# Kernel tuning notes

Measured on AMD Instinct MI355X. Metric: run time of the kernel, lower is better.

Reference implementation:

```python
import jax, jax.numpy as jnp
import numpy as np

DIM = 128   # EMBED_DIM
NH = 4      # N_HEADS
HD = DIM // NH          # 32
NT = max(1, int(NH * 0.25))  # 1 timelike head
NS = NH - NT                 # 3 spacelike heads
TD = NT * HD                 # T_DIM = 32
SD = 6      # STATE_DIM
TIN, TOUT = 20, 20
NL = 3      # N_LAYERS
B, T = 4096, TIN + TOUT      # seq len capped by pos embedding (40)


def _ln(x, g, b):
    m = jnp.mean(x, -1, keepdims=True)
    v = jnp.mean((x - m) ** 2, -1, keepdims=True)
    return g * (x - m) * jax.lax.rsqrt(v + 1e-5) + b


def _mln(x, pg, pb, g, b):
    # MinkowskiLN: standard LN then scale by |sum(s^2)-sum(t^2)| norm
    x = _ln(x, pg, pb)
    t = x[..., :TD]
    s = x[..., TD:]
    mq = jnp.sum(s * s, -1, keepdims=True) - jnp.sum(t * t, -1, keepdims=True)
    eps = jnp.maximum(0.01 * jnp.mean(jnp.abs(mq)), 1e-5)
    return g * (x / (jnp.sqrt(jnp.abs(mq) + eps) + eps)) + b


def _attn(h, qt, kt, qs, ks, vw, ow, ob, ws):
    # Minkowski attention (mode='f3'): timelike scores negated with learned sigmoid weight
    Bb, Tt, _ = h.shape
    scale = HD ** -0.5
    Qt = (h @ qt).reshape(Bb, Tt, NT, HD)
    Kt = (h @ kt).reshape(Bb, Tt, NT, HD)
    Qs = (h @ qs).reshape(Bb, Tt, NS, HD)
    Ks = (h @ ks).reshape(Bb, Tt, NS, HD)
    st = jnp.einsum('bthd,bshd->bths', Qt, Kt)  # [B,T,NT,T]
    ss = jnp.einsum('bthd,bshd->bths', Qs, Ks)  # [B,T,NS,T]
    score = jnp.concatenate([-jax.nn.sigmoid(ws) * st, ss], axis=2) * scale
    a = jax.nn.softmax(score, axis=-1)
    V = (h @ vw).reshape(Bb, Tt, NH, HD)
    o = jnp.einsum('bths,bshd->bthd', a, V).reshape(Bb, Tt, DIM)
    return o @ ow + ob


def setup_inputs() -> dict:
    key = jax.random.key(0)
    ks = iter(jax.random.split(key, 32))
    def w(shape, s=0.02):
        return (jax.random.normal(next(ks), shape, jnp.float32) * s).astype(jnp.float32)
    inp = {
        'x': jax.random.normal(next(ks), (B, T, SD), jnp.float32),
        'embed_w': w((SD, DIM)), 'embed_b': jnp.zeros((DIM,), jnp.float32),
        'pos': w((TIN + TOUT, DIM)),
        'qt_w': w((NL, DIM, NT * HD)), 'kt_w': w((NL, DIM, NT * HD)),
        'qs_w': w((NL, DIM, NS * HD)), 'ks_w': w((NL, DIM, NS * HD)),
        'v_w': w((NL, DIM, DIM)), 'out_w': w((NL, DIM, DIM)), 'out_b': jnp.zeros((NL, DIM), jnp.float32),
        'w_sigma': jnp.zeros((NL,), jnp.float32),
        'n1_pre_g': jnp.ones((NL, DIM), jnp.float32), 'n1_pre_b': jnp.zeros((NL, DIM), jnp.float32),
        'n1_g': jnp.ones((NL, DIM), jnp.float32), 'n1_b': jnp.zeros((NL, DIM), jnp.float32),
        'n2_pre_g': jnp.ones((NL, DIM), jnp.float32), 'n2_pre_b': jnp.zeros((NL, DIM), jnp.float32),
        'n2_g': jnp.ones((NL, DIM), jnp.float32), 'n2_b': jnp.zeros((NL, DIM), jnp.float32),
        'ff_w1': w((NL, DIM, 4 * DIM)), 'ff_b1': jnp.zeros((NL, 4 * DIM), jnp.float32),
        'ff_w2': w((NL, 4 * DIM, DIM)), 'ff_b2': jnp.zeros((NL, DIM), jnp.float32),
        'fn_pre_g': jnp.ones((DIM,), jnp.float32), 'fn_pre_b': jnp.zeros((DIM,), jnp.float32),
        'fn_g': jnp.ones((DIM,), jnp.float32), 'fn_b': jnp.zeros((DIM,), jnp.float32),
        'traj_w': w((DIM, SD * TOUT)), 'traj_b': jnp.zeros((SD * TOUT,), jnp.float32),
    }
    return inp


def reference(x, embed_w, embed_b, pos, qt_w, kt_w, qs_w, ks_w, v_w, out_w, out_b,
              w_sigma, n1_pre_g, n1_pre_b, n1_g, n1_b, n2_pre_g, n2_pre_b, n2_g, n2_b,
              ff_w1, ff_b1, ff_w2, ff_b2, fn_pre_g, fn_pre_b, fn_g, fn_b, traj_w, traj_b):
    Tt = x.shape[1]
    h = x @ embed_w + embed_b + pos[:Tt]  # [B,T,D]
    for i in range(NL):
        h = h + _attn(_mln(h, n1_pre_g[i], n1_pre_b[i], n1_g[i], n1_b[i]),
                      qt_w[i], kt_w[i], qs_w[i], ks_w[i], v_w[i], out_w[i], out_b[i], w_sigma[i])
        hn = _mln(h, n2_pre_g[i], n2_pre_b[i], n2_g[i], n2_b[i])
        h = h + (jax.nn.gelu(hn @ ff_w1[i] + ff_b1[i], approximate=False) @ ff_w2[i] + ff_b2[i])
    h = _mln(h, fn_pre_g, fn_pre_b, fn_g, fn_b)[:, -1, :]  # [B,D]
    out = h @ traj_w + traj_b
    return out.reshape(x.shape[0], TOUT, SD)
```

## Files before the change

kernel.cpp:

```cpp
#include <hip/hip_runtime.h>
#include <hip/hip_bf16.h>

#define DIMM 128
#define TT   40
#define BB   4096
#define NTOK (BB*TT)
#define NLAY 3

typedef float f4 __attribute__((ext_vector_type(4)));
typedef float f32x4 __attribute__((ext_vector_type(4)));
typedef short bf16x8 __attribute__((ext_vector_type(8)));

__device__ __forceinline__ float bf2f(unsigned short u) {
    union { unsigned int i; float f; } v; v.i = ((unsigned int)u) << 16; return v.f;
}
__device__ __forceinline__ unsigned short f2bu(float f) {
    __hip_bfloat16 h = __float2bfloat16(f);
    return *reinterpret_cast<unsigned short*>(&h);
}
__device__ __forceinline__ float gelu_f(float v) {
    float z = 1.5957691216057308f * fmaf(0.044715f * v * v, v, v);
    return v / (1.f + __expf(-z));
}

__device__ __forceinline__ void mln_rowstat(
    const float* v, const float* pgv, const float* pbv,
    float& m, float& rstd, float& mq)
{
    float s1 = 0.f, s2 = 0.f;
    #pragma unroll
    for (int nf = 0; nf < 8; ++nf) { s1 += v[nf]; s2 += v[nf]*v[nf]; }
    #pragma unroll
    for (int o = 1; o < 16; o <<= 1) { s1 += __shfl_xor(s1, o); s2 += __shfl_xor(s2, o); }
    m = s1 * (1.f/128.f);
    float var = s2 * (1.f/128.f) - m*m;
    rstd = rsqrtf(fmaxf(var, 0.f) + 1e-5f);
    float q = 0.f;
    #pragma unroll
    for (int nf = 0; nf < 8; ++nf) {
        float yv = (v[nf] - m) * rstd * pgv[nf] + pbv[nf];
        q += (nf < 2 ? -(yv*yv) : (yv*yv));
    }
    #pragma unroll
    for (int o = 1; o < 16; o <<= 1) q += __shfl_xor(q, o);
    mq = q;
}

__device__ __forceinline__ void build_mln_frags(
    bf16x8 a[2][4], const float* __restrict__ h, int row_mf0, int row_mf1,
    const float* __restrict__ stats, float eps,
    const float* __restrict__ pg, const float* __restrict__ pb,
    const float* __restrict__ gg, const float* __restrict__ gb, int q)
{
    int rows[2] = { row_mf0, row_mf1 };
    float rss3[2], mm[2], s3v[2];
    #pragma unroll
    for (int mf = 0; mf < 2; ++mf) {
        int r = rows[mf];
        float m  = stats[(size_t)r*4 + 0];
        float rs = stats[(size_t)r*4 + 1];
        float mq = stats[(size_t)r*4 + 2];
        float s3 = 1.f / (sqrtf(fabsf(mq) + eps) + eps);
        rss3[mf] = rs * s3; mm[mf] = -m * rss3[mf]; s3v[mf] = s3;
    }
    #pragma unroll
    for (int ks = 0; ks < 4; ++ks) {
        int c0 = ks*32 + q*8;
        float al[8], be[8], gbv[8];
        #pragma unroll
        for (int j = 0; j < 8; ++j) {
            float g = gg[c0+j];
            al[j] = g * pg[c0+j]; be[j] = g * pb[c0+j]; gbv[j] = gb[c0+j];
        }
        #pragma unroll
        for (int mf = 0; mf < 2; ++mf) {
            int r = rows[mf];
            f4 x0 = *(const f4*)(h + (size_t)r*128 + c0);
            f4 x1 = *(const f4*)(h + (size_t)r*128 + c0 + 4);
            union { unsigned short u[8]; bf16x8 v; } o;
            #pragma unroll
            for (int j = 0; j < 4; ++j) {
                float t0 = fmaf(x0[j], rss3[mf], mm[mf]);
                float t1 = fmaf(x1[j], rss3[mf], mm[mf]);
                o.u[j]   = f2bu(fmaf(al[j],   t0, fmaf(be[j],   s3v[mf], gbv[j])));
                o.u[j+4] = f2bu(fmaf(al[j+4], t1, fmaf(be[j+4], s3v[mf], gbv[j+4])));
            }
            a[mf][ks] = o.v;
        }
    }
}

__global__ __launch_bounds__(256) void pack_w_k(
    const float* __restrict__ qt, const float* __restrict__ kt,
    const float* __restrict__ qs, const float* __restrict__ ks,
    const float* __restrict__ vw, const float* __restrict__ ow,
    const float* __restrict__ w1, const float* __restrict__ w2,
    unsigned short* __restrict__ wqT, unsigned short* __restrict__ outT,
    unsigned short* __restrict__ ff1T, unsigned short* __restrict__ ff2T)
{
    int idx = blockIdx.x * 256 + threadIdx.x;
    if (idx < 147456) {
        int i = idx / 49152, r = idx % 49152;
        int n = r / 128, k = r % 128;
        float v;
        if (n < 32)        v = qt[i*4096  + k*32  + n];
        else if (n < 64)   v = kt[i*4096  + k*32  + (n-32)];
        else if (n < 160)  v = qs[i*12288 + k*96  + (n-64)];
        else if (n < 256)  v = ks[i*12288 + k*96  + (n-160)];
        else               v = vw[i*16384 + k*128 + (n-256)];
        wqT[idx] = f2bu(v);
    } else if (idx < 196608) {
        int j = idx - 147456;
        int i = j / 16384, r = j % 16384;
        int n = r / 128, k = r % 128;
        outT[j] = f2bu(ow[i*16384 + k*128 + n]);
    } else if (idx < 393216) {
        int j = idx - 196608;
        int i = j / 65536, r = j % 65536;
        int n = r / 128, k = r % 128;
        ff1T[j] = f2bu(w1[i*65536 + k*512 + n]);
    } else {
        int j = idx - 393216;
        int i = j / 65536, r = j % 65536;
        int n = r / 512, k = r % 512;
        ff2T[j] = f2bu(w2[i*65536 + k*128 + n]);
    }
}

__global__ __launch_bounds__(256) void embed_stats_k(
    const float* __restrict__ x, const float* __restrict__ ew,
    const float* __restrict__ eb, const float* __restrict__ pos,
    const float* __restrict__ pg, const float* __restrict__ pb,
    float* __restrict__ h, float* __restrict__ stats, float* __restrict__ partials)
{
    int wid = threadIdx.x >> 6, lane = threadIdx.x & 63;
    int tok = blockIdx.x * 4 + wid;
    int t = tok % TT;
    const float* xr = x + (size_t)tok * 6;
    float xv[6];
    #pragma unroll
    for (int k = 0; k < 6; ++k) xv[k] = xr[k];
    int d0 = lane, d1 = lane + 64;
    float x0 = eb[d0] + pos[t*128 + d0];
    float x1 = eb[d1] + pos[t*128 + d1];
    #pragma unroll
    for (int k = 0; k < 6; ++k) {
        x0 += xv[k] * ew[k*128 + d0];
        x1 += xv[k] * ew[k*128 + d1];
    }
    h[(size_t)tok*128 + d0] = x0;
    h[(size_t)tok*128 + d1] = x1;

    float s = x0 + x1;
    #pragma unroll
    for (int o = 32; o > 0; o >>= 1) s += __shfl_xor(s, o);
    float m = s * (1.f / 128.f);
    float e0 = x0 - m, e1 = x1 - m;
    float v = e0*e0 + e1*e1;
    #pragma unroll
    for (int o = 32; o > 0; o >>= 1) v += __shfl_xor(v, o);
    float rstd = rsqrtf(v * (1.f / 128.f) + 1e-5f);
    float y0 = e0 * rstd * pg[lane]      + pb[lane];
    float y1 = e1 * rstd * pg[lane + 64] + pb[lane + 64];
    float q = (lane < 32 ? -(y0*y0) : (y0*y0)) + y1*y1;
    #pragma unroll
    for (int o = 32; o > 0; o >>= 1) q += __shfl_xor(q, o);
    if (lane == 0) {
        stats[(size_t)tok*4 + 0] = m;
        stats[(size_t)tok*4 + 1] = rstd;
        stats[(size_t)tok*4 + 2] = q;
    }
    __shared__ float pm[4];
    if (lane == 0) pm[wid] = fabsf(q);
    __syncthreads();
    if (threadIdx.x == 0) partials[blockIdx.x] = (pm[0] + pm[1]) + (pm[2] + pm[3]);
}

__global__ __launch_bounds__(1024) void reduce_eps_k(
    const float* __restrict__ partials, int n, float* __restrict__ scal)
{
    float s = 0.f;
    for (int i = threadIdx.x; i < n; i += 1024) s += partials[i];
    __shared__ float sm[1024];
    sm[threadIdx.x] = s;
    __syncthreads();
    for (int o = 512; o > 0; o >>= 1) {
        if (threadIdx.x < o) sm[threadIdx.x] += sm[threadIdx.x + o];
        __syncthreads();
    }
    if (threadIdx.x == 0) {
        float mean = sm[0] / (float)NTOK;
        scal[0] = fmaxf(0.01f * mean, 1e-5f);
    }
}

__global__ __launch_bounds__(256) void qkv_k(
    const float* __restrict__ hsrc,
    const float* __restrict__ stats_in, const float* __restrict__ scal,
    const float* __restrict__ pg, const float* __restrict__ pb,
    const float* __restrict__ gg, const float* __restrict__ gb,
    const unsigned short* __restrict__ BT,
    unsigned short* __restrict__ obuf)
{
    __shared__ unsigned char Wl[32768];
    const int tid = threadIdx.x, wid = tid >> 6, lane = tid & 63;
    const int q = lane >> 4, l15 = lane & 15;
    const int row0 = blockIdx.x * 128;
    const int wrow = row0 + wid * 32;

    bf16x8 a[2][4];
    build_mln_frags(a, hsrc, wrow + l15, wrow + 16 + l15,
                    stats_in, scal[0], pg, pb, gg, gb, q);

    const unsigned char* BTb = (const unsigned char*)BT;
    for (int nc = 0; nc < 3; ++nc) {
        __syncthreads();
        {
            int row = tid >> 1, half = tid & 1;
            #pragma unroll
            for (int jj = 0; jj < 8; ++jj) {
                int colb = half*128 + jj*16;
                uint4 v = *(const uint4*)(BTb + (size_t)(nc*128 + row)*256 + colb);
                *(uint4*)(Wl + row*256 + (colb ^ ((row & 7) << 4))) = v;
            }
        }
        __syncthreads();
        f32x4 acc[2][8] = {};
        #pragma unroll
        for (int ks = 0; ks < 4; ++ks)
            #pragma unroll
            for (int nf = 0; nf < 8; ++nf) {
                int row = nf*16 + l15;
                bf16x8 b = *(const bf16x8*)(Wl + row*256 + ((ks*64 + q*16) ^ ((row & 7) << 4)));
                #pragma unroll
                for (int mf = 0; mf < 2; ++mf)
                    acc[mf][nf] = __builtin_amdgcn_mfma_f32_16x16x32_bf16(a[mf][ks], b, acc[mf][nf], 0, 0, 0);
            }
        #pragma unroll
        for (int mf = 0; mf < 2; ++mf)
            #pragma unroll
            for (int r = 0; r < 4; ++r) {
                int row = wrow + mf*16 + q*4 + r;
                #pragma unroll
                for (int nf = 0; nf < 8; ++nf)
                    obuf[(size_t)row*384 + nc*128 + nf*16 + l15] = f2bu(acc[mf][nf][r]);
            }
    }
}

__global__ __launch_bounds__(256) void attn_k(
    const unsigned short* __restrict__ scratch, const float* __restrict__ wsp,
    const unsigned short* __restrict__ outT,
    const float* __restrict__ bias,
    float* __restrict__ hres,
    const float* __restrict__ pre_g, const float* __restrict__ pre_b,
    float* __restrict__ stats, float* __restrict__ partials)
{
    __shared__ unsigned char lds[45056];
    __shared__ float sm[16];
    const int b = blockIdx.x, tid = threadIdx.x;
    const unsigned short* base = scratch + (size_t)b * TT * 384;

    unsigned char* VtL = lds;
    unsigned char* PlL = lds + 16384;

    for (int e = tid; e < 1536; e += 256) {
        int hh = e / 384, rem = e - hh*384;
        int row = rem >> 3, c = rem & 7;
        int byte = hh*6144 + ((row*128 + 96 + 4*c) ^ ((row & 7) << 4));
        *(unsigned int*)(PlL + byte) = 0u;
    }
    for (int e = tid; e < 1536; e += 256) {
        int hh = e / 384, rem = e - hh*384;
        int d = rem / 12, sc2 = rem - d*12;
        int s = 40 + 2*sc2;
        int byte = hh*4096 + ((d*128 + s*2) ^ (((d >> 3) & 7) << 4));
        *(unsigned int*)(VtL + byte) = 0u;
    }
    for (int e = tid; e < 640; e += 256) {
        int s = e >> 4, ck = e & 15;
        union { bf16x8 v; unsigned short u[8]; } g;
        g.v = *(const bf16x8*)(base + (size_t)s*384 + 256 + ck*8);
        int hh = ck >> 2, d0 = (ck & 3) * 8;
        #pragma unroll
        for (int j = 0; j < 8; ++j) {
            int d = d0 + j;
            int byte = hh*4096 + ((d*128 + s*2) ^ (((d >> 3) & 7) << 4));
            *(unsigned short*)(VtL + byte) = g.u[j];
        }
    }
    __syncthreads();

    const int h = tid >> 6, lane = tid & 63;
    const int l15 = lane & 15, q4 = lane >> 4;
    const unsigned char* Vt = VtL + h*4096;
    unsigned char* Pl = PlL + h*6144;

    const int qcol = (h == 0) ? 0  : 32  + h*32;
    const int kcol = (h == 0) ? 32 : 128 + h*32;
    const float scale = 0.17677669529663687f;
    const float wmul = (h == 0) ? (-scale / (1.f + __expf(-wsp[0]))) : scale;

    bf16x8 aq[3], bk[3];
    #pragma unroll
    for (int mt = 0; mt < 3; ++mt) {
        int t = l15 + 16*mt; if (t > 39) t = 39;
        aq[mt] = *(const bf16x8*)(base + (size_t)t*384 + qcol + q4*8);
    }
    #pragma unroll
    for (int jt = 0; jt < 3; ++jt) {
        int s = l15 + 16*jt; if (s > 39) s = 39;
        bk[jt] = *(const bf16x8*)(base + (size_t)s*384 + kcol + q4*8);
    }
    f32x4 sc[3][3] = {};
    #pragma unroll
    for (int mt = 0; mt < 3; ++mt)
        #pragma unroll
        for (int jt = 0; jt < 3; ++jt)
            sc[mt][jt] = __builtin_amdgcn_mfma_f32_16x16x32_bf16(aq[mt], bk[jt], sc[mt][jt], 0, 0, 0);

    const bool mask2 = (l15 >= 8);
    float inv[3][4];
    #pragma unroll
    for (int mt = 0; mt < 3; ++mt) {
        #pragma unroll
        for (int r = 0; r < 4; ++r) {
            float s0 = wmul * sc[mt][0][r];
            float s1 = wmul * sc[mt][1][r];
            float s2 = mask2 ? -1e30f : wmul * sc[mt][2][r];
            float mx = fmaxf(fmaxf(s0, s1), s2);
            #pragma unroll
            for (int o = 1; o < 16; o <<= 1) mx = fmaxf(mx, __shfl_xor(mx, o));
            float e0 = __expf(s0 - mx), e1 = __expf(s1 - mx), e2 = __expf(s2 - mx);
            float sum = e0 + e1 + e2;
            #pragma unroll
            for (int o = 1; o < 16; o <<= 1) sum += __shfl_xor(sum, o);
            inv[mt][r] = 1.f / sum;
            int row = 16*mt + 4*q4 + r;
            int rsw = (row & 7) << 4;
            *(unsigned short*)(Pl + ((row*128 + l15*2       ) ^ rsw)) = f2bu(e0);
            *(unsigned short*)(Pl + ((row*128 + 32 + l15*2  ) ^ rsw)) = f2bu(e1);
            *(unsigned short*)(Pl + ((row*128 + 64 + l15*2  ) ^ rsw)) = f2bu(e2);
        }
    }

    f32x4 oacc[3][2] = {};
    #pragma unroll
    for (int ks2 = 0; ks2 < 2; ++ks2) {
        bf16x8 bv[2];
        #pragma unroll
        for (int nt = 0; nt < 2; ++nt) {
            int d = l15 + 16*nt;
            bv[nt] = *(const bf16x8*)(Vt + ((d*128 + 64*ks2 + 16*q4) ^ (((d >> 3) & 7) << 4)));
        }
        #pragma unroll
        for (int mt = 0; mt < 3; ++mt) {
            int row = l15 + 16*mt;
            bf16x8 pa = *(const bf16x8*)(Pl + ((row*128 + 64*ks2 + 16*q4) ^ ((row & 7) << 4)));
            #pragma unroll
            for (int nt = 0; nt < 2; ++nt)
                oacc[mt][nt] = __builtin_amdgcn_mfma_f32_16x16x32_bf16(pa, bv[nt], oacc[mt][nt], 0, 0, 0);
        }
    }

    __syncthreads();
    unsigned char* Ol = lds;
    unsigned char* Wl = lds + 12288;

    #pragma unroll
    for (int mt = 0; mt < 3; ++mt) {
        #pragma unroll
        for (int r = 0; r < 4; ++r) {
            int row = 16*mt + 4*q4 + r;
            float iv = inv[mt][r];
            int rsw = (row & 7) << 4;
            #pragma unroll
            for (int nt = 0; nt < 2; ++nt) {
                int colb = (h*32 + nt*16 + l15) * 2;
                *(unsigned short*)(Ol + ((row*256 + colb) ^ rsw)) = f2bu(oacc[mt][nt][r] * iv);
            }
        }
    }
    {
        const unsigned char* BTb = (const unsigned char*)outT;
        int row = tid >> 1, half = tid & 1;
        #pragma unroll
        for (int jj = 0; jj < 8; ++jj) {
            int colb = half*128 + jj*16;
            uint4 v = *(const uint4*)(BTb + (size_t)row*256 + colb);
            *(uint4*)(Wl + row*256 + (colb ^ ((row & 7) << 4))) = v;
        }
    }
    if (h == 3 && l15 == 0) sm[12 + q4] = 0.f;
    __syncthreads();

    if (h < 3) {
        int arow = 16*h + l15;
        bf16x8 ao[4];
        #pragma unroll
        for (int ks = 0; ks < 4; ++ks)
            ao[ks] = *(const bf16x8*)(Ol + arow*256 + ((ks*64 + q4*16) ^ ((arow & 7) << 4)));
        f32x4 oc[8] = {};
        #pragma unroll
        for (int ks = 0; ks < 4; ++ks)
            #pragma unroll
            for (int nf = 0; nf < 8; ++nf) {
                int brow = nf*16 + l15;
                bf16x8 bo = *(const bf16x8*)(Wl + brow*256 + ((ks*64 + q4*16) ^ ((brow & 7) << 4)));
                oc[nf] = __builtin_amdgcn_mfma_f32_16x16x32_bf16(ao[ks], bo, oc[nf], 0, 0, 0);
            }

        float bv[8], pgv[8], pbv[8];
        #pragma unroll
        for (int nf = 0; nf < 8; ++nf) {
            int c = nf*16 + l15;
            bv[nf] = bias[c]; pgv[nf] = pre_g[c]; pbv[nf] = pre_b[c];
        }
        float amq = 0.f;
        #pragma unroll
        for (int r = 0; r < 4; ++r) {
            int t = 16*h + 4*q4 + r;
            if (t < 40) {
                int row = b*TT + t;
                float* hr = hres + (size_t)row*128;
                float v[8];
                #pragma unroll
                for (int nf = 0; nf < 8; ++nf) {
                    float hv = hr[nf*16 + l15] + oc[nf][r] + bv[nf];
                    hr[nf*16 + l15] = hv;
                    v[nf] = hv;
                }
                float m, rstd, mq;
                mln_rowstat(v, pgv, pbv, m, rstd, mq);
                if (l15 == 0) {
                    stats[(size_t)row*4 + 0] = m;
                    stats[(size_t)row*4 + 1] = rstd;
                    stats[(size_t)row*4 + 2] = mq;
                }
                amq += fabsf(mq);
            }
        }
        if (l15 == 0) sm[h*4 + q4] = amq;
    }
    __syncthreads();
    if (tid == 0) {
        float s = 0.f;
        #pragma unroll
        for (int j = 0; j < 16; ++j) s += sm[j];
        partials[b] = s;
    }
}

__global__ __launch_bounds__(256) void ffn_k(
    const float* __restrict__ hsrc,
    const float* __restrict__ stats_in, const float* __restrict__ scal,
    const float* __restrict__ m2_pre_g, const float* __restrict__ m2_pre_b,
    const float* __restrict__ m2_g, const float* __restrict__ m2_b,
    const unsigned short* __restrict__ W1T,
    const float* __restrict__ b1,
    const unsigned short* __restrict__ W2T,
    const float* __restrict__ b2,
    float* __restrict__ h,
    const float* __restrict__ pre_g, const float* __restrict__ pre_b,
    float* __restrict__ stats, float* __restrict__ partials)
{
    __shared__ unsigned char W1l[16384];
    __shared__ unsigned char W2l[16384];
    __shared__ unsigned char Ps[4][32*144];
    __shared__ float sm[16];
    const int tid = threadIdx.x, wid = tid >> 6, lane = tid & 63;
    const int q = lane >> 4, l15 = lane & 15;
    const int row0 = blockIdx.x * 128;
    const int wrow = row0 + wid * 32;
    unsigned char* Pw = Ps[wid];

    bf16x8 a[2][4];
    build_mln_frags(a, hsrc, wrow + l15, wrow + 16 + l15,
                    stats_in, scal[0], m2_pre_g, m2_pre_b, m2_g, m2_b, q);

    float b2v[8];
    #pragma unroll
    for (int nf = 0; nf < 8; ++nf) b2v[nf] = b2[nf*16 + l15];

    f32x4 acc2[2][8] = {};
    const unsigned char* W1b = (const unsigned char*)W1T;
    const unsigned char* W2b = (const unsigned char*)W2T;

    for (int c = 0; c < 8; ++c) {
        __syncthreads();
        {
            int row = tid >> 2, seg = tid & 3;
            #pragma unroll
            for (int jj = 0; jj < 4; ++jj) {
                int colb = seg*64 + jj*16;
                uint4 v = *(const uint4*)(W1b + (size_t)(c*64 + row)*256 + colb);
                *(uint4*)(W1l + row*256 + (colb ^ ((row & 7) << 4))) = v;
            }
        }
        {
            int row = tid >> 1, seg = tid & 1;
            #pragma unroll
            for (int jj = 0; jj < 4; ++jj) {
                int colb = seg*64 + jj*16;
                uint4 v = *(const uint4*)(W2b + (size_t)row*1024 + c*128 + colb);
                *(uint4*)(W2l + row*128 + (colb ^ ((row & 7) << 4))) = v;
            }
        }
        __syncthreads();
        float bbv[4];
        #pragma unroll
        for (int nf = 0; nf < 4; ++nf) bbv[nf] = b1[c*64 + nf*16 + l15];
        f32x4 acc1[2][4];
        #pragma unroll
        for (int mf = 0; mf < 2; ++mf)
            #pragma unroll
            for (int nf = 0; nf < 4; ++nf)
                acc1[mf][nf] = f32x4{bbv[nf], bbv[nf], bbv[nf], bbv[nf]};
        #pragma unroll
        for (int ks = 0; ks < 4; ++ks)
            #pragma unroll
            for (int nf = 0; nf < 4; ++nf) {
                int row = nf*16 + l15;
                bf16x8 b = *(const bf16x8*)(W1l + row*256 + ((ks*64 + q*16) ^ ((row & 7) << 4)));
                #pragma unroll
                for (int mf = 0; mf < 2; ++mf)
                    acc1[mf][nf] = __builtin_amdgcn_mfma_f32_16x16x32_bf16(a[mf][ks], b, acc1[mf][nf], 0, 0, 0);
            }
        #pragma unroll
        for (int nf = 0; nf < 4; ++nf) {
            #pragma unroll
            for (int mf = 0; mf < 2; ++mf) {
                #pragma unroll
                for (int r = 0; r < 4; ++r) {
                    float v = gelu_f(acc1[mf][nf][r]);
                    *(unsigned short*)(Pw + (mf*16 + q*4 + r)*144 + (nf*16 + l15)*2) = f2bu(v);
                }
            }
        }
        #pragma unroll
        for (int ks2 = 0; ks2 < 2; ++ks2) {
            bf16x8 a2[2];
            #pragma unroll
            for (int mf = 0; mf < 2; ++mf)
                a2[mf] = *(const bf16x8*)(Pw + (mf*16 + l15)*144 + ks2*64 + q*16);
            #pragma unroll
            for (int nf = 0; nf < 8; ++nf) {
                int row = nf*16 + l15;
                bf16x8 b = *(const bf16x8*)(W2l + row*128 + ((ks2*64 + q*16) ^ ((row & 7) << 4)));
                #pragma unroll
                for (int mf = 0; mf < 2; ++mf)
                    acc2[mf][nf] = __builtin_amdgcn_mfma_f32_16x16x32_bf16(a2[mf], b, acc2[mf][nf], 0, 0, 0);
            }
        }
    }

    float pgv[8], pbv[8];
    #pragma unroll
    for (int nf = 0; nf < 8; ++nf) { pgv[nf] = pre_g[nf*16 + l15]; pbv[nf] = pre_b[nf*16 + l15]; }
    float amq = 0.f;
    #pragma unroll
    for (int mf = 0; mf < 2; ++mf) {
        #pragma unroll
        for (int r = 0; r < 4; ++r) {
            int row = wrow + mf*16 + q*4 + r;
            float* hr = h + (size_t)row*128;
            float v[8];
            #pragma unroll
            for (int nf = 0; nf < 8; ++nf) {
                float hv = hr[nf*16 + l15] + acc2[mf][nf][r] + b2v[nf];
                hr[nf*16 + l15] = hv;
                v[nf] = hv;
            }
            float m, rstd, mq;
            mln_rowstat(v, pgv, pbv, m, rstd, mq);
            if (l15 == 0) {
                stats[(size_t)row*4 + 0] = m;
                stats[(size_t)row*4 + 1] = rstd;
                stats[(size_t)row*4 + 2] = mq;
            }
            amq += fabsf(mq);
        }
    }
    if (l15 == 0) sm[wid*4 + q] = amq;
    __syncthreads();
    if (tid == 0) {
        float s = 0.f;
        #pragma unroll
        for (int j = 0; j < 16; ++j) s += sm[j];
        partials[blockIdx.x] = s;
    }
}

__global__ __launch_bounds__(128) void head_k(
    const float* __restrict__ h, const float* __restrict__ stats, const float* __restrict__ scal,
    const float* __restrict__ pg, const float* __restrict__ pb,
    const float* __restrict__ gg, const float* __restrict__ gb,
    const float* __restrict__ tw, const float* __restrict__ tb,
    float* __restrict__ out)
{
    int b = blockIdx.x, tid = threadIdx.x;
    int tok = b*TT + (TT - 1);
    __shared__ float ys[128];
    float eps = scal[0];
    float m  = stats[(size_t)tok*4 + 0];
    float rs = stats[(size_t)tok*4 + 1];
    float mq = stats[(size_t)tok*4 + 2];
    float s3 = 1.f / (sqrtf(fabsf(mq) + eps) + eps);
    float x = h[(size_t)tok*128 + tid];
    ys[tid] = gg[tid] * (((x - m) * rs * pg[tid] + pb[tid]) * s3) + gb[tid];
    __syncthreads();
    if (tid < 120) {
        float acc = tb[tid];
        #pragma unroll 4
        for (int d = 0; d < 128; ++d) acc += ys[d] * tw[d*120 + tid];
        out[(size_t)b*120 + tid] = acc;
    }
}

extern "C" void kernel_launch(void* const* d_in, const int* in_sizes, int n_in,
                              void* d_out, int out_size, void* d_ws, size_t ws_size,
                              hipStream_t stream) {
    const float* x        = (const float*)d_in[0];
    const float* embed_w  = (const float*)d_in[1];
    const float* embed_b  = (const float*)d_in[2];
    const float* pos      = (const float*)d_in[3];
    const float* qt_w     = (const float*)d_in[4];
    const float* kt_w     = (const float*)d_in[5];
    const float* qs_w     = (const float*)d_in[6];
    const float* ks_w     = (const float*)d_in[7];
    const float* v_w      = (const float*)d_in[8];
    const float* out_w    = (const float*)d_in[9];
    const float* out_b    = (const float*)d_in[10];
    const float* w_sigma  = (const float*)d_in[11];
    const float* n1_pre_g = (const float*)d_in[12];
    const float* n1_pre_b = (const float*)d_in[13];
    const float* n1_g     = (const float*)d_in[14];
    const float* n1_b     = (const float*)d_in[15];
    const float* n2_pre_g = (const float*)d_in[16];
    const float* n2_pre_b = (const float*)d_in[17];
    const float* n2_g     = (const float*)d_in[18];
    const float* n2_b     = (const float*)d_in[19];
    const float* ff_w1    = (const float*)d_in[20];
    const float* ff_b1    = (const float*)d_in[21];
    const float* ff_w2    = (const float*)d_in[22];
    const float* ff_b2    = (const float*)d_in[23];
    const float* fn_pre_g = (const float*)d_in[24];
    const float* fn_pre_b = (const float*)d_in[25];
    const float* fn_g     = (const float*)d_in[26];
    const float* fn_b     = (const float*)d_in[27];
    const float* traj_w   = (const float*)d_in[28];
    const float* traj_b   = (const float*)d_in[29];

    char* ws = (char*)d_ws;
    float*          h        = (float*)ws;
    float*          stats    = (float*)(ws + 83886080);
    unsigned short* scratch  = (unsigned short*)(ws + 86507520);
    unsigned short* wqT      = (unsigned short*)(ws + 212336640);
    unsigned short* outT     = (unsigned short*)(ws + 212631552);
    unsigned short* ff1T     = (unsigned short*)(ws + 212729856);
    unsigned short* ff2T     = (unsigned short*)(ws + 213123072);
    float*          partials = (float*)(ws + 213516288);
    float*          scal     = (float*)(ws + 213680128);

    pack_w_k<<<2304, 256, 0, stream>>>(qt_w, kt_w, qs_w, ks_w, v_w, out_w, ff_w1, ff_w2,
                                       wqT, outT, ff1T, ff2T);
    embed_stats_k<<<40960, 256, 0, stream>>>(x, embed_w, embed_b, pos,
                                             n1_pre_g, n1_pre_b, h, stats, partials);
    reduce_eps_k<<<1, 1024, 0, stream>>>(partials, 40960, scal);

    for (int i = 0; i < NLAY; ++i) {
        qkv_k<<<1280, 256, 0, stream>>>(
            h, stats, scal,
            n1_pre_g + i*128, n1_pre_b + i*128, n1_g + i*128, n1_b + i*128,
            wqT + (size_t)i*49152, scratch);
        attn_k<<<4096, 256, 0, stream>>>(
            scratch, w_sigma + i,
            outT + (size_t)i*16384, out_b + i*128,
            h, n2_pre_g + i*128, n2_pre_b + i*128,
            stats, partials);
        reduce_eps_k<<<1, 1024, 0, stream>>>(partials, 4096, scal);
        const float* npg = (i < NLAY-1) ? (n1_pre_g + (i+1)*128) : fn_pre_g;
        const float* npb = (i < NLAY-1) ? (n1_pre_b + (i+1)*128) : fn_pre_b;
        ffn_k<<<1280, 256, 0, stream>>>(
            h, stats, scal,
            n2_pre_g + i*128, n2_pre_b + i*128, n2_g + i*128, n2_b + i*128,
            ff1T + (size_t)i*65536, ff_b1 + i*512,
            ff2T + (size_t)i*65536, ff_b2 + i*128, h,
            npg, npb, stats, partials);
        reduce_eps_k<<<1, 1024, 0, stream>>>(partials, 1280, scal);
    }

    head_k<<<4096, 128, 0, stream>>>(h, stats, scal, fn_pre_g, fn_pre_b, fn_g, fn_b,
                                     traj_w, traj_b, (float*)d_out);
}
```

Measured before the change: 870.5 us.

## Split FFN block work across eight waves of sixteen rows each

The FFN kernel now launches 512 threads per block, so eight waves each handle 16 rows instead of four waves handling 32 rows. The per-wave MFMA tiles, the GELU staging buffer and the LDS weight-loading pattern are reworked to match. The intent is more waves per block to hide latency and a lower register footprint per thread. In exchange, each B fragment loaded from LDS is reused across only one M tile instead of two, which doubles LDS weight reads per MFMA, and more waves contend at the barriers.

Result: faster. 812.5 us (median of 5 runs) (-6.7%).

```diff
diff --git a/kernel.cpp b/kernel.cpp
--- a/kernel.cpp
+++ b/kernel.cpp
@@ -87,6 +87,35 @@
             }
             a[mf][ks] = o.v;
         }
+    }
+}
+
+__device__ __forceinline__ void build_mln_frags1(
+    bf16x8 a[4], const float* __restrict__ h, int row,
+    const float* __restrict__ stats, float eps,
+    const float* __restrict__ pg, const float* __restrict__ pb,
+    const float* __restrict__ gg, const float* __restrict__ gb, int q)
+{
+    float m  = stats[(size_t)row*4 + 0];
+    float rs = stats[(size_t)row*4 + 1];
+    float mq = stats[(size_t)row*4 + 2];
+    float s3 = 1.f / (sqrtf(fabsf(mq) + eps) + eps);
+    float rss3 = rs * s3, mm = -m * rss3;
+    #pragma unroll
+    for (int ks = 0; ks < 4; ++ks) {
+        int c0 = ks*32 + q*8;
+        f4 x0 = *(const f4*)(h + (size_t)row*128 + c0);
+        f4 x1 = *(const f4*)(h + (size_t)row*128 + c0 + 4);
+        union { unsigned short u[8]; bf16x8 v; } o;
+        #pragma unroll
+        for (int j = 0; j < 4; ++j) {
+            float g0 = gg[c0+j], g1 = gg[c0+j+4];
+            float t0 = fmaf(x0[j], rss3, mm);
+            float t1 = fmaf(x1[j], rss3, mm);
+            o.u[j]   = f2bu(fmaf(g0 * pg[c0+j],   t0, fmaf(g0 * pb[c0+j],   s3, gb[c0+j])));
+            o.u[j+4] = f2bu(fmaf(g1 * pg[c0+j+4], t1, fmaf(g1 * pb[c0+j+4], s3, gb[c0+j+4])));
+        }
+        a[ks] = o.v;
     }
 }
 
@@ -451,7 +480,7 @@
     }
 }
 
-__global__ __launch_bounds__(256) void ffn_k(
+__global__ __launch_bounds__(512) void ffn_k(
     const float* __restrict__ hsrc,
     const float* __restrict__ stats_in, const float* __restrict__ scal,
     const float* __restrict__ m2_pre_g, const float* __restrict__ m2_pre_b,
@@ -466,42 +495,42 @@
 {
     __shared__ unsigned char W1l[16384];
     __shared__ unsigned char W2l[16384];
-    __shared__ unsigned char Ps[4][32*144];
-    __shared__ float sm[16];
+    __shared__ unsigned char Ps[8][16*144];
+    __shared__ float sm[32];
     const int tid = threadIdx.x, wid = tid >> 6, lane = tid & 63;
     const int q = lane >> 4, l15 = lane & 15;
     const int row0 = blockIdx.x * 128;
-    const int wrow = row0 + wid * 32;
+    const int wrow = row0 + wid * 16;
     unsigned char* Pw = Ps[wid];
 
-    bf16x8 a[2][4];
-    build_mln_frags(a, hsrc, wrow + l15, wrow + 16 + l15,
-                    stats_in, scal[0], m2_pre_g, m2_pre_b, m2_g, m2_b, q);
+    bf16x8 a[4];
+    build_mln_frags1(a, hsrc, wrow + l15,
+                     stats_in, scal[0], m2_pre_g, m2_pre_b, m2_g, m2_b, q);
 
     float b2v[8];
     #pragma unroll
     for (int nf = 0; nf < 8; ++nf) b2v[nf] = b2[nf*16 + l15];
 
-    f32x4 acc2[2][8] = {};
+    f32x4 acc2[8] = {};
     const unsigned char* W1b = (const unsigned char*)W1T;
     const unsigned char* W2b = (const unsigned char*)W2T;
 
     for (int c = 0; c < 8; ++c) {
         __syncthreads();
         {
-            int row = tid >> 2, seg = tid & 3;
-            #pragma unroll
-            for (int jj = 0; jj < 4; ++jj) {
-                int colb = seg*64 + jj*16;
+            int row = tid >> 3, seg = tid & 7;
+            #pragma unroll
+            for (int jj = 0; jj < 2; ++jj) {
+                int colb = seg*32 + jj*16;
                 uint4 v = *(const uint4*)(W1b + (size_t)(c*64 + row)*256 + colb);
                 *(uint4*)(W1l + row*256 + (colb ^ ((row & 7) << 4))) = v;
             }
         }
         {
-            int row = tid >> 1, seg = tid & 1;
-            #pragma unroll
-            for (int jj = 0; jj < 4; ++jj) {
-                int colb = seg*64 + jj*16;
+            int row = tid >> 2, seg = tid & 3;
+            #pragma unroll
+            for (int jj = 0; jj < 2; ++jj) {
+                int colb = seg*32 + jj*16;
                 uint4 v = *(const uint4*)(W2b + (size_t)row*1024 + c*128 + colb);
                 *(uint4*)(W2l + row*128 + (colb ^ ((row & 7) << 4))) = v;
             }
@@ -510,46 +539,34 @@
         float bbv[4];
         #pragma unroll
         for (int nf = 0; nf < 4; ++nf) bbv[nf] = b1[c*64 + nf*16 + l15];
-        f32x4 acc1[2][4];
-        #pragma unroll
-        for (int mf = 0; mf < 2; ++mf)
-            #pragma unroll
-            for (int nf = 0; nf < 4; ++nf)
-                acc1[mf][nf] = f32x4{bbv[nf], bbv[nf], bbv[nf], bbv[nf]};
+        f32x4 acc1[4];
+        #pragma unroll
+        for (int nf = 0; nf < 4; ++nf)
+            acc1[nf] = f32x4{bbv[nf], bbv[nf], bbv[nf], bbv[nf]};
         #pragma unroll
         for (int ks = 0; ks < 4; ++ks)
             #pragma unroll
             for (int nf = 0; nf < 4; ++nf) {
                 int row = nf*16 + l15;
                 bf16x8 b = *(const bf16x8*)(W1l + row*256 + ((ks*64 + q*16) ^ ((row & 7) << 4)));
-                #pragma unroll
-                for (int mf = 0; mf < 2; ++mf)
-                    acc1[mf][nf] = __builtin_amdgcn_mfma_f32_16x16x32_bf16(a[mf][ks], b, acc1[mf][nf], 0, 0, 0);
+                acc1[nf] = __builtin_amdgcn_mfma_f32_16x16x32_bf16(a[ks], b, acc1[nf], 0, 0, 0);
             }
         #pragma unroll
         for (int nf = 0; nf < 4; ++nf) {
             #pragma unroll
-            for (int mf = 0; mf < 2; ++mf) {
-                #pragma unroll
-                for (int r = 0; r < 4; ++r) {
-                    float v = gelu_f(acc1[mf][nf][r]);
-                    *(unsigned short*)(Pw + (mf*16 + q*4 + r)*144 + (nf*16 + l15)*2) = f2bu(v);
-                }
+            for (int r = 0; r < 4; ++r) {
+                float v = gelu_f(acc1[nf][r]);
+                *(unsigned short*)(Pw + (q*4 + r)*144 + (nf*16 + l15)*2) = f2bu(v);
             }
         }
         #pragma unroll
         for (int ks2 = 0; ks2 < 2; ++ks2) {
-            bf16x8 a2[2];
-            #pragma unroll
-            for (int mf = 0; mf < 2; ++mf)
-                a2[mf] = *(const bf16x8*)(Pw + (mf*16 + l15)*144 + ks2*64 + q*16);
+            bf16x8 a2 = *(const bf16x8*)(Pw + l15*144 + ks2*64 + q*16);
             #pragma unroll
             for (int nf = 0; nf < 8; ++nf) {
                 int row = nf*16 + l15;
                 bf16x8 b = *(const bf16x8*)(W2l + row*128 + ((ks2*64 + q*16) ^ ((row & 7) << 4)));
-                #pragma unroll
-                for (int mf = 0; mf < 2; ++mf)
-                    acc2[mf][nf] = __builtin_amdgcn_mfma_f32_16x16x32_bf16(a2[mf], b, acc2[mf][nf], 0, 0, 0);
+                acc2[nf] = __builtin_amdgcn_mfma_f32_16x16x32_bf16(a2, b, acc2[nf], 0, 0, 0);
             }
         }
     }
@@ -559,34 +576,31 @@
     for (int nf = 0; nf < 8; ++nf) { pgv[nf] = pre_g[nf*16 + l15]; pbv[nf] = pre_b[nf*16 + l15]; }
     float amq = 0.f;
     #pragma unroll
-    for (int mf = 0; mf < 2; ++mf) {
-        #pragma unroll
-        for (int r = 0; r < 4; ++r) {
-            int row = wrow + mf*16 + q*4 + r;
-            float* hr = h + (size_t)row*128;
-            float v[8];
-            #pragma unroll
-            for (int nf = 0; nf < 8; ++nf) {
-                float hv = hr[nf*16 + l15] + acc2[mf][nf][r] + b2v[nf];
-                hr[nf*16 + l15] = hv;
-                v[nf] = hv;
-            }
-            float m, rstd, mq;
-            mln_rowstat(v, pgv, pbv, m, rstd, mq);
-            if (l15 == 0) {
-                stats[(size_t)row*4 + 0] = m;
-                stats[(size_t)row*4 + 1] = rstd;
-                stats[(size_t)row*4 + 2] = mq;
-            }
-            amq += fabsf(mq);
-        }
+    for (int r = 0; r < 4; ++r) {
+        int row = wrow + q*4 + r;
+        float* hr = h + (size_t)row*128;
+        float v[8];
+        #pragma unroll
+        for (int nf = 0; nf < 8; ++nf) {
+            float hv = hr[nf*16 + l15] + acc2[nf][r] + b2v[nf];
+            hr[nf*16 + l15] = hv;
+            v[nf] = hv;
+        }
+        float m, rstd, mq;
+        mln_rowstat(v, pgv, pbv, m, rstd, mq);
+        if (l15 == 0) {
+            stats[(size_t)row*4 + 0] = m;
+            stats[(size_t)row*4 + 1] = rstd;
+            stats[(size_t)row*4 + 2] = mq;
+        }
+        amq += fabsf(mq);
     }
     if (l15 == 0) sm[wid*4 + q] = amq;
     __syncthreads();
     if (tid == 0) {
         float s = 0.f;
         #pragma unroll
-        for (int j = 0; j < 16; ++j) s += sm[j];
+        for (int j = 0; j < 32; ++j) s += sm[j];
         partials[blockIdx.x] = s;
     }
 }
@@ -681,7 +695,7 @@
         reduce_eps_k<<<1, 1024, 0, stream>>>(partials, 4096, scal);
         const float* npg = (i < NLAY-1) ? (n1_pre_g + (i+1)*128) : fn_pre_g;
         const float* npb = (i < NLAY-1) ? (n1_pre_b + (i+1)*128) : fn_pre_b;
-        ffn_k<<<1280, 256, 0, stream>>>(
+        ffn_k<<<1280, 512, 0, stream>>>(
             h, stats, scal,
             n2_pre_g + i*128, n2_pre_b + i*128, n2_g + i*128, n2_b + i*128,
             ff1T + (size_t)i*65536, ff_b1 + i*512,
```
